# Kernel optimization log

Measured on AMD Instinct MI355X. Metric: run time of the kernel, lower is better.

Reference implementation:

```python
import jax, jax.numpy as jnp
import numpy as np


def setup_inputs() -> dict:
    key = jax.random.key(0)
    k1, k2, k3 = jax.random.split(key, 3)
    B, N, D = 16, 512, 256
    # integer frame durations per token, 4..11 frames (avg ~7.5)
    durations = jax.random.randint(k1, (B, N), 4, 12, dtype=jnp.int32)
    # T = max over batch of total frames (static python int, mirrors torch.arange(0, max(s)))
    total_len = int(jnp.max(jnp.sum(durations, axis=-1)))
    x = jax.random.normal(k2, (B, N, D), dtype=jnp.float32)
    # positive Gaussian range (std) per token
    ranges = jax.random.uniform(k3, (B, N), minval=0.5, maxval=4.0, dtype=jnp.float32)
    return {"x": x, "durations": durations, "ranges": ranges, "total_len": total_len}


def _gaussian_weights(durations, ranges, total_len):
    # e: cumulative end frame per token, c: Gaussian center per token
    e = jnp.cumsum(durations, axis=-1).astype(jnp.float32)          # [B, N]
    c = (e - 0.5 * durations.astype(jnp.float32))[..., None]        # [B, N, 1]
    t = jnp.arange(total_len, dtype=jnp.float32)[None, None, :]     # [1, 1, T]
    inv_r2 = ranges[..., None] ** (-2)                               # [B, N, 1]
    w1 = jnp.exp(-inv_r2 * (t - c) ** 2)                             # [B, N, T]
    # original computes the exp twice (w_1 and inside w_2); same math, computed once
    w2 = jnp.sum(w1, axis=1, keepdims=True) + 1e-20                  # [B, 1, T]
    return w1 / w2


def _create_positions(durations, total_len):
    # frame-index-within-token positions: pos[b, t] = t - start_of_segment(t)
    e = jnp.cumsum(durations, axis=-1)                               # [B, N]
    starts = e - durations                                           # [B, N]
    t = jnp.arange(total_len, dtype=durations.dtype)                 # [T]
    seg = jax.vmap(lambda eb: jnp.searchsorted(eb, t, side='right'))(e)  # [B, T]
    seg = jnp.clip(seg, 0, durations.shape[-1] - 1)
    return t[None, :] - jnp.take_along_axis(starts, seg, axis=-1)    # [B, T]


def reference(x, durations, ranges, total_len):
    weights = _gaussian_weights(durations, ranges, total_len)        # [B, N, T]
    # matmul(weights.transpose(1,2), x) -> [B, T, D]
    out = jnp.einsum('bnt,bnd->btd', weights, x)
    positions = _create_positions(durations, total_len)
    return positions, out, weights
```

## Files before the change

### kernel.cpp

```cpp
#include <hip/hip_runtime.h>
#include <hip/hip_bf16.h>


#define TT  64
#define NWC 44
#define WBS 72
#define MARGIN 42.0f

#define SCB 16
#define XPB 512
#define ZFB 2048

typedef __attribute__((ext_vector_type(8))) short short8;
typedef __attribute__((ext_vector_type(8))) unsigned short ushort8;
typedef __attribute__((ext_vector_type(4))) float f32x4;

__device__ inline unsigned short f2bf(float f) {
    union { float f; unsigned int u; } v; v.f = f;
    unsigned int u = v.u;
    return (unsigned short)((u + 0x7FFFu + ((u >> 16) & 1u)) >> 16);
}

__global__ __launch_bounds__(512) void k1_combo(
        const float* __restrict__ x, const int* __restrict__ dur,
        const float* __restrict__ ranges,
        unsigned short* __restrict__ xT,
        float* __restrict__ c, float* __restrict__ ir,
        int* __restrict__ e_i, int* __restrict__ st_i,
        float* __restrict__ out2, int T) {
    const int N = 512;
    int bid = blockIdx.x, tid = threadIdx.x;

    __shared__ unsigned short tile[64][72];
    __shared__ int wsum[8], woff[8];

    if (bid < SCB) {
        int b = bid;
        int lane = tid & 63, wid = tid >> 6;
        int d = dur[b * N + tid];
        int v = d;
        #pragma unroll
        for (int off = 1; off < 64; off <<= 1) {
            int t = __shfl_up(v, off);
            if (lane >= off) v += t;
        }
        if (lane == 63) wsum[wid] = v;
        __syncthreads();
        if (tid == 0) { int a = 0; for (int i = 0; i < 8; i++) { woff[i] = a; a += wsum[i]; } }
        __syncthreads();
        int e = v + woff[wid];
        float r = ranges[b * N + tid];
        c[b * N + tid]    = (float)e - 0.5f * (float)d;
        ir[b * N + tid]   = 1.0f / (r * r);
        e_i[b * N + tid]  = e;
        st_i[b * N + tid] = e - d;
    } else if (bid < SCB + XPB) {
        int v = bid - SCB;
        int bx = v & 7, by = (v >> 3) & 3, b = v >> 5;
        int n0 = bx * 64, d0 = by * 64;
        const float* xb = x + ((size_t)b * 512 + n0) * 256 + d0;
        int dl = tid & 63, ng = tid >> 6;
        #pragma unroll
        for (int i = 0; i < 8; i++) {
            int nl = ng * 8 + i;
            tile[nl][dl] = f2bf(xb[(size_t)nl * 256 + dl]);
        }
        __syncthreads();
        unsigned short* xTb = xT + (size_t)b * 131072;
        int ci  = tid;
        int l15 = ci & 15;
        int sub = ci >> 4;
        int tkb = sub & 7, dkb = sub >> 3;
        ushort8 vv;
        #pragma unroll
        for (int k = 0; k < 8; k++) vv[k] = tile[tkb * 8 + k][dkb * 16 + l15];
        *(ushort8*)(xTb + ((((by * 4 + dkb) * 64) + bx * 8 + tkb) << 7)
                        + (l15 << 3)) = vv;
    } else {
        const f32x4 z4 = (f32x4){0.f, 0.f, 0.f, 0.f};
        f32x4* p = (f32x4*)out2;
        size_t nv4 = (size_t)2048 * (size_t)T;
        size_t stride = (size_t)ZFB * 512;
        for (size_t i = (size_t)(bid - SCB - XPB) * 512 + tid; i < nv4; i += stride)
            p[i] = z4;
    }
}

__global__ __launch_bounds__(256) void pass1_kernel(
        const unsigned short* __restrict__ xT, const float* __restrict__ c,
        const float* __restrict__ ir,
        const int* __restrict__ e_i, const int* __restrict__ st_i,
        float* __restrict__ pos_out ,
        float* __restrict__ out1 ,
        float* __restrict__ out2 ,
        int T) {
    const int N = 512;
    const int D = 256;
    int b = blockIdx.y;
    int t0 = blockIdx.x * TT;
    int tid = threadIdx.x;

    __shared__ float c_s[512];
    __shared__ float ir_s[512];
    __shared__ int   es[512], ss[512];
    __shared__ __align__(16) unsigned short wb[TT][WBS];
    __shared__ float part[4][TT];
    __shared__ float iw2_s[TT];
    __shared__ int lohi[2];

    for (int i = tid; i < 512; i += 256) {
        c_s[i]  = c[b * N + i];
        ir_s[i] = ir[b * N + i];
        es[i]   = e_i[b * N + i];
        ss[i]   = st_i[b * N + i];
    }
    __syncthreads();

    if (tid == 0) {
        float lo_v = (float)t0 - MARGIN;
        float hi_v = (float)(t0 + TT - 1) + MARGIN;
        int lo = 0, hi = 512;
        while (lo < hi) { int m = (lo + hi) >> 1; if (c_s[m] < lo_v) lo = m + 1; else hi = m; }
        int l = lo;
        lo = 0; hi = 512;
        while (lo < hi) { int m = (lo + hi) >> 1; if (c_s[m] <= hi_v) lo = m + 1; else hi = m; }
        int h = lo - 1;
        if (h > l + NWC - 1) h = l + NWC - 1;
        l &= ~7;
        if (l > 448) l = 448;
        lohi[0] = l; lohi[1] = h;
    }
    if (tid < TT) {
        int t = t0 + tid;
        if (t < T) {
            int lo = 0, hi = 512;
            while (lo < hi) { int m = (lo + hi) >> 1; if (es[m] <= t) lo = m + 1; else hi = m; }
            int seg = min(lo, 511);
            pos_out[b * T + t] = (float)(t - ss[seg]);
        }
    }
    __syncthreads();
    int lo_u = lohi[0], hi_u = lohi[1];

    int tl = tid & 63;
    int s  = tid >> 6;
    int t  = t0 + tl;

    ushort8 wv0, wv1;
    float p = 0.f;
    #pragma unroll
    for (int jj = 0; jj < 16; jj++) {
        int n = lo_u + 16 * s + jj;
        float w1 = 0.f;
        if (n <= hi_u && t < T) {
            float dd = (float)t - c_s[n];
            w1 = expf(-ir_s[n] * dd * dd);
        }
        unsigned short hb = f2bf(w1);
        if (jj < 8) wv0[jj] = hb; else wv1[jj - 8] = hb;
        p += w1;
    }
    *(ushort8*)&wb[tl][16 * s]     = wv0;
    *(ushort8*)&wb[tl][16 * s + 8] = wv1;
    part[s][tl] = p;
    __syncthreads();
    if (tid < TT) {
        float w2 = part[0][tid] + part[1][tid] + part[2][tid] + part[3][tid];
        iw2_s[tid] = 1.0f / (w2 + 1e-20f);
    }
    __syncthreads();

    int lane = tid & 63;
    int l15  = lane & 15;
    int q    = lane >> 4;

    f32x4 acc[4][4];
    #pragma unroll
    for (int mt = 0; mt < 4; mt++)
        #pragma unroll
        for (int nt = 0; nt < 4; nt++)
            acc[mt][nt] = (f32x4){0.f, 0.f, 0.f, 0.f};

    const unsigned short* xTb = xT + (size_t)b * 131072;
    #pragma unroll
    for (int ks = 0; ks < 2; ks++) {
        int tokb = (lo_u >> 3) + ks * 4 + q;
        short8 afrag[4];
        #pragma unroll
        for (int mt = 0; mt < 4; mt++)
            afrag[mt] = *(const short8*)&wb[16 * mt + l15][ks * 32 + q * 8];
        #pragma unroll
        for (int nt = 0; nt < 4; nt++) {
            int dblk = 4 * s + nt;
            short8 bfrag = *(const short8*)(xTb + (((dblk << 6) + tokb) << 7) + (l15 << 3));
            #pragma unroll
            for (int mt = 0; mt < 4; mt++)
                acc[mt][nt] = __builtin_amdgcn_mfma_f32_16x16x32_bf16(afrag[mt], bfrag, acc[mt][nt], 0, 0, 0);
        }
    }

    #pragma unroll
    for (int mt = 0; mt < 4; mt++) {
        #pragma unroll
        for (int r = 0; r < 4; r++) {
            int tt = t0 + 16 * mt + q * 4 + r;
            if (tt < T) {
                float iw2 = iw2_s[16 * mt + q * 4 + r];
                float* orow = out1 + ((size_t)b * T + tt) * D + 64 * s;
                #pragma unroll
                for (int nt = 0; nt < 4; nt++)
                    orow[nt * 16 + l15] = acc[mt][nt][r] * iw2;
            }
        }
    }

    if (t < T) {
        float iw2l = iw2_s[tl];
        int nw = hi_u - lo_u + 1;
        for (int i = s; i < nw; i += 4) {
            int n = lo_u + i;
            float dd = (float)t - c_s[n];
            float w = expf(-ir_s[n] * dd * dd) * iw2l;
            out2[((size_t)b * N + n) * (size_t)T + t] = w;
        }
    }
}

extern "C" void kernel_launch(void* const* d_in, const int* in_sizes, int n_in,
                              void* d_out, int out_size, void* d_ws, size_t ws_size,
                              hipStream_t stream) {
    const float* x      = (const float*)d_in[0];
    const int*   dur    = (const int*)d_in[1];
    const float* ranges = (const float*)d_in[2];
    const int B = 16, N = 512, D = 256;
    const int T = out_size / (B * (1 + D + N));

    float* pos_out = (float*)d_out;
    float* out1    = pos_out + (size_t)B * T;
    float* out2    = out1 + (size_t)B * T * D;

    float* c      = (float*)d_ws;
    float* ir     = c + B * N;
    int*   e_i    = (int*)(ir + B * N);
    int*   st_i   = e_i + B * N;
    unsigned short* xT = (unsigned short*)(st_i + B * N);

    k1_combo<<<SCB + XPB + ZFB, 512, 0, stream>>>(x, dur, ranges, xT,
                                                  c, ir, e_i, st_i, out2, T);

    dim3 g1((T + TT - 1) / TT, B);
    pass1_kernel<<<g1, 256, 0, stream>>>(xT, c, ir, e_i, st_i,
                                         pos_out, out1, out2, T);
}
```

Baseline: 211.6 us.

## Move out2 zero-fill into main kernel and skip the Gaussian band

```diff
diff --git a/kernel.cpp b/kernel.cpp
--- a/kernel.cpp
+++ b/kernel.cpp
@@ -9,7 +9,7 @@
 
 #define SCB 16
 #define XPB 512
-#define ZFB 2048
+#define FB  2048
 
 typedef __attribute__((ext_vector_type(8))) short short8;
 typedef __attribute__((ext_vector_type(8))) unsigned short ushort8;
@@ -21,13 +21,12 @@
     return (unsigned short)((u + 0x7FFFu + ((u >> 16) & 1u)) >> 16);
 }
 
-__global__ __launch_bounds__(512) void k1_combo(
+__global__ __launch_bounds__(512) void k0_prep(
         const float* __restrict__ x, const int* __restrict__ dur,
         const float* __restrict__ ranges,
         unsigned short* __restrict__ xT,
         float* __restrict__ c, float* __restrict__ ir,
-        int* __restrict__ e_i, int* __restrict__ st_i,
-        float* __restrict__ out2, int T) {
+        int* __restrict__ e_i, int* __restrict__ st_i) {
     const int N = 512;
     int bid = blockIdx.x, tid = threadIdx.x;
 
@@ -54,7 +53,7 @@
         ir[b * N + tid]   = 1.0f / (r * r);
         e_i[b * N + tid]  = e;
         st_i[b * N + tid] = e - d;
-    } else if (bid < SCB + XPB) {
+    } else {
         int v = bid - SCB;
         int bx = v & 7, by = (v >> 3) & 3, b = v >> 5;
         int n0 = bx * 64, d0 = by * 64;
@@ -76,29 +75,21 @@
         for (int k = 0; k < 8; k++) vv[k] = tile[tkb * 8 + k][dkb * 16 + l15];
         *(ushort8*)(xTb + ((((by * 4 + dkb) * 64) + bx * 8 + tkb) << 7)
                         + (l15 << 3)) = vv;
-    } else {
-        const f32x4 z4 = (f32x4){0.f, 0.f, 0.f, 0.f};
-        f32x4* p = (f32x4*)out2;
-        size_t nv4 = (size_t)2048 * (size_t)T;
-        size_t stride = (size_t)ZFB * 512;
-        for (size_t i = (size_t)(bid - SCB - XPB) * 512 + tid; i < nv4; i += stride)
-            p[i] = z4;
-    }
-}
-
-__global__ __launch_bounds__(256) void pass1_kernel(
+    }
+}
+
+__global__ __launch_bounds__(256) void k1_main(
         const unsigned short* __restrict__ xT, const float* __restrict__ c,
         const float* __restrict__ ir,
         const int* __restrict__ e_i, const int* __restrict__ st_i,
         float* __restrict__ pos_out ,
         float* __restrict__ out1 ,
         float* __restrict__ out2 ,
-        int T) {
+        int T, int ntiles) {
     const int N = 512;
     const int D = 256;
-    int b = blockIdx.y;
-    int t0 = blockIdx.x * TT;
-    int tid = threadIdx.x;
+    int bid = blockIdx.x, tid = threadIdx.x;
+    int NP = ntiles * 16;
 
     __shared__ float c_s[512];
     __shared__ float ir_s[512];
@@ -107,6 +98,50 @@
     __shared__ float part[4][TT];
     __shared__ float iw2_s[TT];
     __shared__ int lohi[2];
+
+    if (bid >= NP) {
+        int fid = bid - NP;
+        const f32x4 z4 = (f32x4){0.f, 0.f, 0.f, 0.f};
+        for (int r = 0; r < 4; r++) {
+            int g = fid * 4 + r;
+            int b = g >> 9, n = g & 511;
+            float cn = c[b * N + n];
+            int zl = (int)ceilf(cn - 42.0f);
+            if (zl < 0) zl = 0; if (zl > T) zl = T;
+            int zh = (int)(cn + 42.0f) + 1;
+            if (zh > T) zh = T; if (zh < zl) zh = zl;
+            size_t base = ((size_t)b * N + n) * (size_t)T;
+            int head = (int)((4 - (base & 3)) & 3);
+            if (head > T) head = T;
+            if (tid < head) {
+                int t = tid;
+                if (t < zl || t >= zh) out2[base + t] = 0.f;
+            }
+            int ngrp = (T - head) >> 2;
+            int tail = (T - head) & 3;
+            float* rowp = (float*)(out2 + base + head);
+            for (int gg = tid; gg < ngrp; gg += 256) {
+                int tg = head + 4 * gg;
+                if (tg + 3 < zl || tg >= zh) {
+                    *(f32x4*)(rowp + 4 * gg) = z4;
+                } else if (tg < zl || tg + 3 >= zh) {
+                    #pragma unroll
+                    for (int k = 0; k < 4; k++) {
+                        int t = tg + k;
+                        if (t < zl || t >= zh) rowp[4 * gg + k] = 0.f;
+                    }
+                }
+            }
+            if (tid < tail) {
+                int t = head + 4 * ngrp + tid;
+                if (t < zl || t >= zh) out2[base + t] = 0.f;
+            }
+        }
+        return;
+    }
+
+    int b  = bid / ntiles;
+    int t0 = (bid - b * ntiles) * TT;
 
     for (int i = tid; i < 512; i += 256) {
         c_s[i]  = c[b * N + i];
@@ -245,10 +280,9 @@
     int*   st_i   = e_i + B * N;
     unsigned short* xT = (unsigned short*)(st_i + B * N);
 
-    k1_combo<<<SCB + XPB + ZFB, 512, 0, stream>>>(x, dur, ranges, xT,
-                                                  c, ir, e_i, st_i, out2, T);
-
-    dim3 g1((T + TT - 1) / TT, B);
-    pass1_kernel<<<g1, 256, 0, stream>>>(xT, c, ir, e_i, st_i,
-                                         pos_out, out1, out2, T);
-}
+    k0_prep<<<SCB + XPB, 512, 0, stream>>>(x, dur, ranges, xT, c, ir, e_i, st_i);
+
+    int ntiles = (T + TT - 1) / TT;
+    k1_main<<<ntiles * 16 + FB, 256, 0, stream>>>(xT, c, ir, e_i, st_i,
+                                                  pos_out, out1, out2, T, ntiles);
+}
```

New measurement: 209.8 us. No clear change (-0.9%).
